# Optimization experiments

Hardware: AMD Instinct MI355X
Metric: run time of the kernel (lower is better)

Reference implementation:

```python
import jax, jax.numpy as jnp
import numpy as np

V, D, NH, L, T, B = 32000, 1024, 16, 6, 1024, 2
HS = D // NH
EPS = 1e-5


def setup_inputs() -> dict:
    key = jax.random.key(0)
    ks = jax.random.split(key, 20)
    s = 0.02
    inp = {
        'tokens': jax.random.randint(ks[0], (B, T), 0, V),
        'tok_emb': jax.random.normal(ks[1], (V, D), jnp.float32) * s,
        'pos_emb': jax.random.normal(ks[2], (T, D), jnp.float32) * s,
        'Wq': jax.random.normal(ks[3], (L, D, NH, HS), jnp.float32) * s,
        'Wk': jax.random.normal(ks[4], (L, D, NH, HS), jnp.float32) * s,
        'Wv': jax.random.normal(ks[5], (L, D, NH, HS), jnp.float32) * s,
        'Wo': jax.random.normal(ks[6], (L, D, D), jnp.float32) * s,
        'bo': jnp.zeros((L, D), jnp.float32),
        'ln1_s': jnp.ones((L, D), jnp.float32),
        'ln1_b': jnp.zeros((L, D), jnp.float32),
        'ln2_s': jnp.ones((L, D), jnp.float32),
        'ln2_b': jnp.zeros((L, D), jnp.float32),
        'W1': jax.random.normal(ks[7], (L, D, 4 * D), jnp.float32) * s,
        'b1': jnp.zeros((L, 4 * D), jnp.float32),
        'W2': jax.random.normal(ks[8], (L, 4 * D, D), jnp.float32) * s,
        'b2': jnp.zeros((L, D), jnp.float32),
        'lnf_s': jnp.ones((D,), jnp.float32),
        'lnf_b': jnp.zeros((D,), jnp.float32),
        'Wlm': jax.random.normal(ks[9], (D, V), jnp.float32) * s,
        'blm': jnp.zeros((V,), jnp.float32),
    }
    return inp


def _layernorm(x, scale, bias):
    m = jnp.mean(x, axis=-1, keepdims=True)
    v = jnp.mean(jnp.square(x - m), axis=-1, keepdims=True)
    return (x - m) * jax.lax.rsqrt(v + EPS) * scale + bias


def reference(tokens, tok_emb, pos_emb, Wq, Wk, Wv, Wo, bo,
              ln1_s, ln1_b, ln2_s, ln2_b, W1, b1, W2, b2,
              lnf_s, lnf_b, Wlm, blm):
    x = tok_emb[tokens] + pos_emb[None, :, :]  # [B,T,D]
    causal = jnp.tril(jnp.ones((T, T), bool))
    scale = HS ** -0.5
    for l in range(L):
        h = _layernorm(x, ln1_s[l], ln1_b[l])
        q = jnp.einsum('btd,dhe->bhte', h, Wq[l])
        k = jnp.einsum('btd,dhe->bhte', h, Wk[l])
        v = jnp.einsum('btd,dhe->bhte', h, Wv[l])
        wei = jnp.einsum('bhqe,bhke->bhqk', q, k) * scale
        wei = jnp.where(causal, wei, -jnp.inf)
        wei = jax.nn.softmax(wei, axis=-1)
        attn = jnp.einsum('bhqk,bhke->bhqe', wei, v)  # [B,NH,T,HS]
        attn = attn.transpose(0, 2, 1, 3).reshape(B, T, D)
        x = x + attn @ Wo[l] + bo[l]
        h = _layernorm(x, ln2_s[l], ln2_b[l])
        x = x + jax.nn.relu(h @ W1[l] + b1[l]) @ W2[l] + b2[l]
    x = _layernorm(x, lnf_s, lnf_b)
    logits = x @ Wlm + blm  # [B,T,V]
    return logits
```

## Files before the change

### kernel.cpp

```cpp
#include <hip/hip_runtime.h>
#include <hip/hip_bf16.h>
#include <stdint.h>

#define L_LAYERS 6
#define D_MODEL  1024
#define N_HEAD   16
#define H_SZ     64
#define T_SEQ    1024
#define B_BATCH  2
#define M_ROWS   2048
#define V_VOCAB  32000

typedef __attribute__((ext_vector_type(8))) short bf16x8;
typedef __attribute__((ext_vector_type(4))) short bf16x4;
typedef __attribute__((ext_vector_type(4))) float floatx4;

static __device__ __forceinline__ short f2bf(float f) {
  __hip_bfloat16 h = __float2bfloat16(f);
  return *reinterpret_cast<short*>(&h);
}

static __device__ __forceinline__ void lds_cp16(const void* g, void* l) {
  __builtin_amdgcn_global_load_lds(
      (const __attribute__((address_space(1))) uint32_t*)g,
      (__attribute__((address_space(3))) uint32_t*)l, 16, 0, 0);
}

#define WVM(n) asm volatile("s_waitcnt vmcnt(" #n ")" ::: "memory")
#define BARR __builtin_amdgcn_s_barrier()

__global__ __launch_bounds__(256) void transpose_cvt(const float* __restrict__ in,
                                                     short* __restrict__ out,
                                                     int R, int C,
                                                     long in_stride, long out_stride) {
  in  += (size_t)blockIdx.z * in_stride;
  out += (size_t)blockIdx.z * out_stride;
  __shared__ float tile[64][65];
  int rt = blockIdx.x, ct = blockIdx.y;
  int tid = threadIdx.x;
  int r0 = tid >> 4;
  int c0 = (tid & 15) << 2;
  const float* ip = in + (size_t)(rt * 64) * C + ct * 64;
#pragma unroll
  for (int p = 0; p < 4; ++p) {
    int r = r0 + (p << 4);
    float4 v = *(const float4*)(ip + (size_t)r * C + c0);
    tile[r][c0] = v.x; tile[r][c0 + 1] = v.y; tile[r][c0 + 2] = v.z; tile[r][c0 + 3] = v.w;
  }
  __syncthreads();
  short* op = out + (size_t)(ct * 64) * R + rt * 64;
#pragma unroll
  for (int p = 0; p < 4; ++p) {
    int c = r0 + (p << 4);
    bf16x4 s;
    s.x = f2bf(tile[c0 + 0][c]);
    s.y = f2bf(tile[c0 + 1][c]);
    s.z = f2bf(tile[c0 + 2][c]);
    s.w = f2bf(tile[c0 + 3][c]);
    *(bf16x4*)(op + (size_t)c * R + c0) = s;
  }
}

__global__ __launch_bounds__(256) void embed_kernel(const int* __restrict__ tokens,
                                                    const float* __restrict__ tok_emb,
                                                    const float* __restrict__ pos_emb,
                                                    float* __restrict__ x) {
  int row = blockIdx.x;
  int t = row & 1023;
  int tok = tokens[row];
  int c = threadIdx.x << 2;
  float4 e = *(const float4*)(tok_emb + (size_t)tok * 1024 + c);
  float4 p = *(const float4*)(pos_emb + (size_t)t * 1024 + c);
  float4 rr; rr.x = e.x + p.x; rr.y = e.y + p.y; rr.z = e.z + p.z; rr.w = e.w + p.w;
  *(float4*)(x + (size_t)row * 1024 + c) = rr;
}

__global__ __launch_bounds__(256) void ln_kernel(const float* __restrict__ xin,
                                                 const float* __restrict__ sc,
                                                 const float* __restrict__ bi,
                                                 short* __restrict__ out) {
  int row = blockIdx.x, tid = threadIdx.x;
  int c = tid << 2;
  float4 v = *(const float4*)(xin + (size_t)row * 1024 + c);
  float s = v.x + v.y + v.z + v.w;
  float q = v.x * v.x + v.y * v.y + v.z * v.z + v.w * v.w;
#pragma unroll
  for (int off = 32; off > 0; off >>= 1) {
    s += __shfl_xor(s, off);
    q += __shfl_xor(q, off);
  }
  __shared__ float rs[4], rq[4];
  if ((tid & 63) == 0) { rs[tid >> 6] = s; rq[tid >> 6] = q; }
  __syncthreads();
  s = rs[0] + rs[1] + rs[2] + rs[3];
  q = rq[0] + rq[1] + rq[2] + rq[3];
  float mean = s * (1.f / 1024.f);
  float var = q * (1.f / 1024.f) - mean * mean;
  float rstd = rsqrtf(var + 1e-5f);
  float4 g = *(const float4*)(sc + c);
  float4 bb = *(const float4*)(bi + c);
  bf16x4 o4;
  o4.x = f2bf((v.x - mean) * rstd * g.x + bb.x);
  o4.y = f2bf((v.y - mean) * rstd * g.y + bb.y);
  o4.z = f2bf((v.z - mean) * rstd * g.z + bb.z);
  o4.w = f2bf((v.w - mean) * rstd * g.w + bb.w);
  *(bf16x4*)(out + (size_t)row * 1024 + c) = o4;
}

__global__ __launch_bounds__(256) void lnred_kernel(float* __restrict__ xio,
                                                    const float* __restrict__ P0,
                                                    const float* __restrict__ P1,
                                                    const float* __restrict__ gb,
                                                    const float* __restrict__ sc,
                                                    const float* __restrict__ bi,
                                                    short* __restrict__ out) {
  int row = blockIdx.x, tid = threadIdx.x;
  int c = tid << 2;
  size_t base = (size_t)row * 1024 + c;
  float4 v = *(const float4*)(xio + base);
  float4 p0 = *(const float4*)(P0 + base);
  float4 p1 = *(const float4*)(P1 + base);
  float4 gv = *(const float4*)(gb + c);
  v.x += p0.x + p1.x + gv.x;
  v.y += p0.y + p1.y + gv.y;
  v.z += p0.z + p1.z + gv.z;
  v.w += p0.w + p1.w + gv.w;
  *(float4*)(xio + base) = v;
  float s = v.x + v.y + v.z + v.w;
  float q = v.x * v.x + v.y * v.y + v.z * v.z + v.w * v.w;
#pragma unroll
  for (int off = 32; off > 0; off >>= 1) {
    s += __shfl_xor(s, off);
    q += __shfl_xor(q, off);
  }
  __shared__ float rs[4], rq[4];
  if ((tid & 63) == 0) { rs[tid >> 6] = s; rq[tid >> 6] = q; }
  __syncthreads();
  s = rs[0] + rs[1] + rs[2] + rs[3];
  q = rq[0] + rq[1] + rq[2] + rq[3];
  float mean = s * (1.f / 1024.f);
  float var = q * (1.f / 1024.f) - mean * mean;
  float rstd = rsqrtf(var + 1e-5f);
  float4 g = *(const float4*)(sc + c);
  float4 bb = *(const float4*)(bi + c);
  bf16x4 o4;
  o4.x = f2bf((v.x - mean) * rstd * g.x + bb.x);
  o4.y = f2bf((v.y - mean) * rstd * g.y + bb.y);
  o4.z = f2bf((v.z - mean) * rstd * g.z + bb.z);
  o4.w = f2bf((v.w - mean) * rstd * g.w + bb.w);
  *(bf16x4*)(out + (size_t)row * 1024 + c) = o4;
}

template <bool BIAS, bool RELU, bool RESID, bool OUTBF16>
__global__ __launch_bounds__(256) void gemm3_kernel(const short* __restrict__ A,
                                                    const short* __restrict__ Bt,
                                                    const float* __restrict__ bias,
                                                    const float* __restrict__ resid,
                                                    void* __restrict__ Cout,
                                                    int K, int N) {
  constexpr int ABY = 64 * 128;
  constexpr int BBY = 128 * 128;
  extern __shared__ char smem[];
  char* Asm = smem;
  char* Bsm = smem + 3 * ABY;
  const int NB = N >> 7;
  int nwg = 32 * NB;
  int bid = blockIdx.x;
  int wgid = (bid & 7) * (nwg >> 3) + (bid >> 3);
  int bn = wgid >> 5, bm = wgid & 31;
  int tid = threadIdx.x;
  int lane = tid & 63, w = tid >> 6;
  int lr = lane & 15, lg = lane >> 4;
  int wn = w & 1, wm = w >> 1;

  const floatx4 FZ = {0.f, 0.f, 0.f, 0.f};
  floatx4 acc[2][4];
#pragma unroll
  for (int m = 0; m < 2; ++m)
#pragma unroll
    for (int n = 0; n < 4; ++n) acc[m][n] = FZ;

  size_t aoff[2], boff[4];
  {
    int rr = tid >> 3;
    int g = (tid & 7) ^ (rr & 7);
#pragma unroll
    for (int i = 0; i < 2; ++i)
      aoff[i] = (size_t)(bm * 64 + i * 32 + rr) * K + g * 8;
#pragma unroll
    for (int i = 0; i < 4; ++i)
      boff[i] = (size_t)(bn * 128 + i * 32 + rr) * K + g * 8;
  }

#define STA3(b, k0)                                                        \
  _Pragma("unroll") for (int i = 0; i < 2; ++i)                            \
    lds_cp16(A + aoff[i] + (k0), Asm + (b) * ABY + i * 4096 + tid * 16);
#define STB3(b, k0)                                                        \
  _Pragma("unroll") for (int i = 0; i < 4; ++i)                            \
    lds_cp16(Bt + boff[i] + (k0), Bsm + (b) * BBY + i * 4096 + tid * 16);
#define LDA3(b, kh)                                                        \
  _Pragma("unroll") for (int f = 0; f < 2; ++f) {                          \
    int lrow = wm * 32 + f * 16 + lr;                                      \
    af[f] = *(const bf16x8*)(Asm + (b) * ABY + lrow * 128 +                \
                             (((((kh) << 2) + lg) ^ (lrow & 7)) << 4));    \
  }
#define LDB3(b, kh)                                                        \
  _Pragma("unroll") for (int n = 0; n < 4; ++n) {                          \
    int lcol = wn * 64 + n * 16 + lr;                                      \
    bfr[n] = *(const bf16x8*)(Bsm + (b) * BBY + lcol * 128 +               \
                              (((((kh) << 2) + lg) ^ (lcol & 7)) << 4));   \
  }
#define MFMA3                                                              \
  __builtin_amdgcn_s_setprio(1);                                           \
  _Pragma("unroll") for (int f = 0; f < 2; ++f)                            \
  _Pragma("unroll") for (int n = 0; n < 4; ++n)                            \
    acc[f][n] = __builtin_amdgcn_mfma_f32_16x16x32_bf16(af[f], bfr[n],     \
                                                        acc[f][n], 0, 0, 0);\
  __builtin_amdgcn_s_setprio(0);

  const int nt = K >> 6;
  STA3(0, 0); STB3(0, 0);
  STA3(1, 64); STB3(1, 64);
  WVM(6);
  BARR;

  int cbuf = 0, sbuf = 2;
  for (int t = 0; t < nt; ++t) {
    bf16x8 af[2], bfr[4];
    bool pre = (t + 2 < nt);
    int k2 = (t + 2) << 6;
    if (pre) { STA3(sbuf, k2); }
    LDA3(cbuf, 0); LDB3(cbuf, 0);
    MFMA3;
    if (pre) { STB3(sbuf, k2); }
    LDA3(cbuf, 1); LDB3(cbuf, 1);
    MFMA3;
    if (pre) { WVM(6); } else { WVM(0); }
    BARR;
    cbuf = (cbuf == 2) ? 0 : cbuf + 1;
    sbuf = (sbuf == 2) ? 0 : sbuf + 1;
  }

#pragma unroll
  for (int n = 0; n < 4; ++n) {
    int col = (bn << 7) + wn * 64 + (n << 4) + lr;
    float bv = 0.f;
    if (BIAS) bv = bias[col];
#pragma unroll
    for (int m = 0; m < 2; ++m) {
      int row0 = bm * 64 + wm * 32 + (m << 4) + (lg << 2);
#pragma unroll
      for (int r = 0; r < 4; ++r) {
        size_t idx = (size_t)(row0 + r) * N + col;
        float val = acc[m][n][r] + bv;
        if (RESID) val += resid[idx];
        if (RELU) val = fmaxf(val, 0.f);
        if (OUTBF16) ((short*)Cout)[idx] = f2bf(val);
        else ((float*)Cout)[idx] = val;
      }
    }
  }
#undef STA3
#undef STB3
#undef LDA3
#undef LDB3
#undef MFMA3
}

__global__ __launch_bounds__(256) void gemm3sk_kernel(const short* __restrict__ A,
                                                      const short* __restrict__ Bt,
                                                      float* __restrict__ Pout,
                                                      int K, int N) {
  constexpr int ABY = 64 * 128;
  constexpr int BBY = 128 * 128;
  extern __shared__ char smem[];
  char* Asm = smem;
  char* Bsm = smem + 3 * ABY;
  const int NB = N >> 7;
  int nwg = 64 * NB;
  int bid = blockIdx.x;
  int wgid = (bid & 7) * (nwg >> 3) + (bid >> 3);
  int half = wgid >= (nwg >> 1);
  int w2 = wgid - half * (nwg >> 1);
  int bn = w2 >> 5, bm = w2 & 31;
  int kbase = half * (K >> 1);
  Pout += (size_t)half * M_ROWS * N;
  int tid = threadIdx.x;
  int lane = tid & 63, w = tid >> 6;
  int lr = lane & 15, lg = lane >> 4;
  int wn = w & 1, wm = w >> 1;

  const floatx4 FZ = {0.f, 0.f, 0.f, 0.f};
  floatx4 acc[2][4];
#pragma unroll
  for (int m = 0; m < 2; ++m)
#pragma unroll
    for (int n = 0; n < 4; ++n) acc[m][n] = FZ;

  size_t aoff[2], boff[4];
  {
    int rr = tid >> 3;
    int g = (tid & 7) ^ (rr & 7);
#pragma unroll
    for (int i = 0; i < 2; ++i)
      aoff[i] = (size_t)(bm * 64 + i * 32 + rr) * K + kbase + g * 8;
#pragma unroll
    for (int i = 0; i < 4; ++i)
      boff[i] = (size_t)(bn * 128 + i * 32 + rr) * K + kbase + g * 8;
  }

#define STA3(b, k0)                                                        \
  _Pragma("unroll") for (int i = 0; i < 2; ++i)                            \
    lds_cp16(A + aoff[i] + (k0), Asm + (b) * ABY + i * 4096 + tid * 16);
#define STB3(b, k0)                                                        \
  _Pragma("unroll") for (int i = 0; i < 4; ++i)                            \
    lds_cp16(Bt + boff[i] + (k0), Bsm + (b) * BBY + i * 4096 + tid * 16);
#define LDA3(b, kh)                                                        \
  _Pragma("unroll") for (int f = 0; f < 2; ++f) {                          \
    int lrow = wm * 32 + f * 16 + lr;                                      \
    af[f] = *(const bf16x8*)(Asm + (b) * ABY + lrow * 128 +                \
                             (((((kh) << 2) + lg) ^ (lrow & 7)) << 4));    \
  }
#define LDB3(b, kh)                                                        \
  _Pragma("unroll") for (int n = 0; n < 4; ++n) {                          \
    int lcol = wn * 64 + n * 16 + lr;                                      \
    bfr[n] = *(const bf16x8*)(Bsm + (b) * BBY + lcol * 128 +               \
                              (((((kh) << 2) + lg) ^ (lcol & 7)) << 4));   \
  }
#define MFMA3                                                              \
  __builtin_amdgcn_s_setprio(1);                                           \
  _Pragma("unroll") for (int f = 0; f < 2; ++f)                            \
  _Pragma("unroll") for (int n = 0; n < 4; ++n)                            \
    acc[f][n] = __builtin_amdgcn_mfma_f32_16x16x32_bf16(af[f], bfr[n],     \
                                                        acc[f][n], 0, 0, 0);\
  __builtin_amdgcn_s_setprio(0);

  const int nt = (K >> 1) >> 6;
  STA3(0, 0); STB3(0, 0);
  STA3(1, 64); STB3(1, 64);
  WVM(6);
  BARR;

  int cbuf = 0, sbuf = 2;
  for (int t = 0; t < nt; ++t) {
    bf16x8 af[2], bfr[4];
    bool pre = (t + 2 < nt);
    int k2 = (t + 2) << 6;
    if (pre) { STA3(sbuf, k2); }
    LDA3(cbuf, 0); LDB3(cbuf, 0);
    MFMA3;
    if (pre) { STB3(sbuf, k2); }
    LDA3(cbuf, 1); LDB3(cbuf, 1);
    MFMA3;
    if (pre) { WVM(6); } else { WVM(0); }
    BARR;
    cbuf = (cbuf == 2) ? 0 : cbuf + 1;
    sbuf = (sbuf == 2) ? 0 : sbuf + 1;
  }

#pragma unroll
  for (int n = 0; n < 4; ++n) {
    int col = (bn << 7) + wn * 64 + (n << 4) + lr;
#pragma unroll
    for (int m = 0; m < 2; ++m) {
      int row0 = bm * 64 + wm * 32 + (m << 4) + (lg << 2);
#pragma unroll
      for (int r = 0; r < 4; ++r)
        Pout[(size_t)(row0 + r) * N + col] = acc[m][n][r];
    }
  }
#undef STA3
#undef STB3
#undef LDA3
#undef LDB3
#undef MFMA3
}

template <bool BIAS, bool RELU, bool OUTBF16>
__global__ __launch_bounds__(512) void gemmw_kernel(const short* __restrict__ A,
                                                    const short* __restrict__ Bt,
                                                    const float* __restrict__ bias,
                                                    void* __restrict__ Cout,
                                                    int K, int N) {
  constexpr int ABY = 128 * 128;
  constexpr int BBY = 256 * 128;
  extern __shared__ char smem[];
  char* Asm = smem;
  char* Bsm = smem + 3 * ABY;
  const int NB = N >> 8;
  int nwg = 16 * NB;
  int bid = blockIdx.x;
  int wgid = (bid & 7) * (nwg >> 3) + (bid >> 3);
  int bn = wgid >> 4, bm = wgid & 15;
  int tid = threadIdx.x;
  int lane = tid & 63, w = tid >> 6;
  int lr = lane & 15, lg = lane >> 4;
  int wm = w >> 2, wn = w & 3;

  const floatx4 FZ = {0.f, 0.f, 0.f, 0.f};
  floatx4 acc[4][4];
#pragma unroll
  for (int m = 0; m < 4; ++m)
#pragma unroll
    for (int n = 0; n < 4; ++n) acc[m][n] = FZ;

  size_t aoff[2], boff[4];
  {
    int rr = tid >> 3;
    int g = (tid & 7) ^ (rr & 7);
#pragma unroll
    for (int i = 0; i < 2; ++i)
      aoff[i] = (size_t)(bm * 128 + i * 64 + rr) * K + g * 8;
#pragma unroll
    for (int i = 0; i < 4; ++i)
      boff[i] = (size_t)(bn * 256 + i * 64 + rr) * K + g * 8;
  }

#define STAW(b, k0)                                                        \
  _Pragma("unroll") for (int i = 0; i < 2; ++i)                            \
    lds_cp16(A + aoff[i] + (k0), Asm + (b) * ABY + i * 8192 + tid * 16);
#define STBW(b, k0)                                                        \
  _Pragma("unroll") for (int i = 0; i < 4; ++i)                            \
    lds_cp16(Bt + boff[i] + (k0), Bsm + (b) * BBY + i * 8192 + tid * 16);
#define LDAW(b, kh)                                                        \
  _Pragma("unroll") for (int f = 0; f < 4; ++f) {                          \
    int lrow = wm * 64 + f * 16 + lr;                                      \
    af[f] = *(const bf16x8*)(Asm + (b) * ABY + lrow * 128 +                \
                             (((((kh) << 2) + lg) ^ (lrow & 7)) << 4));    \
  }
#define LDBW(b, kh)                                                        \
  _Pragma("unroll") for (int n = 0; n < 4; ++n) {                          \
    int lcol = wn * 64 + n * 16 + lr;                                      \
    bfr[n] = *(const bf16x8*)(Bsm + (b) * BBY + lcol * 128 +               \
                              (((((kh) << 2) + lg) ^ (lcol & 7)) << 4));   \
  }
#define MFMAW                                                              \
  __builtin_amdgcn_s_setprio(1);                                           \
  _Pragma("unroll") for (int f = 0; f < 4; ++f)                            \
  _Pragma("unroll") for (int n = 0; n < 4; ++n)                            \
    acc[f][n] = __builtin_amdgcn_mfma_f32_16x16x32_bf16(af[f], bfr[n],     \
                                                        acc[f][n], 0, 0, 0);\
  __builtin_amdgcn_s_setprio(0);

  const int nt = K >> 6;
  STAW(0, 0); STBW(0, 0);
  STAW(1, 64); STBW(1, 64);
  WVM(6);
  BARR;

  int cbuf = 0, sbuf = 2;
  for (int t = 0; t < nt; ++t) {
    bf16x8 af[4], bfr[4];
    bool pre = (t + 2 < nt);
    int k2 = (t + 2) << 6;
    if (pre) { STAW(sbuf, k2); }
    LDAW(cbuf, 0); LDBW(cbuf, 0);
    MFMAW;
    if (pre) { STBW(sbuf, k2); }
    LDAW(cbuf, 1); LDBW(cbuf, 1);
    MFMAW;
    if (pre) { WVM(6); } else { WVM(0); }
    BARR;
    cbuf = (cbuf == 2) ? 0 : cbuf + 1;
    sbuf = (sbuf == 2) ? 0 : sbuf + 1;
  }

#pragma unroll
  for (int n = 0; n < 4; ++n) {
    int col = (bn << 8) + wn * 64 + (n << 4) + lr;
    float bv = 0.f;
    if (BIAS) bv = bias[col];
#pragma unroll
    for (int m = 0; m < 4; ++m) {
      int row0 = bm * 128 + wm * 64 + (m << 4) + (lg << 2);
#pragma unroll
      for (int r = 0; r < 4; ++r) {
        size_t idx = (size_t)(row0 + r) * N + col;
        float val = acc[m][n][r] + bv;
        if (RELU) val = fmaxf(val, 0.f);
        if (OUTBF16) ((short*)Cout)[idx] = f2bf(val);
        else ((float*)Cout)[idx] = val;
      }
    }
  }
#undef STAW
#undef STBW
#undef LDAW
#undef LDBW
#undef MFMAW
}

template <bool BIAS, bool OUTBF16>
__global__ __launch_bounds__(512) void gemm8_kernel(const short* __restrict__ A,
                                                    const short* __restrict__ Bt,
                                                    const float* __restrict__ bias,
                                                    void* __restrict__ Cout,
                                                    int K, int N) {
  extern __shared__ char smem[];
  char* Asm = smem;
  char* Bsm = smem + 65536;
  const int NB = N >> 8;
  int nwg = 8 * NB;
  int bid = blockIdx.x;
  int wgid = (bid & 7) * (nwg >> 3) + (bid >> 3);
  int bm = wgid & 7, bn = wgid >> 3;
  int tid = threadIdx.x;
  int lane = tid & 63, w = tid >> 6;
  int lr = lane & 15, lg = lane >> 4;
  int wm = w >> 2, wn = w & 3;

  const floatx4 FZ = {0.f, 0.f, 0.f, 0.f};
  floatx4 acc[8][4];
#pragma unroll
  for (int m = 0; m < 8; ++m)
#pragma unroll
    for (int n = 0; n < 4; ++n) acc[m][n] = FZ;

  size_t aoff[2][2], boff[4];
  {
    int rr = tid >> 3;
    int g = (tid & 7) ^ (rr & 7);
#pragma unroll
    for (int c = 0; c < 2; ++c)
#pragma unroll
      for (int i = 0; i < 2; ++i) {
        int lrow = i * 64 + rr;
        int grow = (lrow & 63) + ((lrow >> 6) << 7) + (c << 6);
        aoff[c][i] = (size_t)(bm * 256 + grow) * K + g * 8;
      }
#pragma unroll
    for (int i = 0; i < 4; ++i)
      boff[i] = (size_t)(bn * 256 + i * 64 + rr) * K + g * 8;
  }

  bf16x8 areg[4], breg[2][4];

#define LDA8(chunk, kh)                                                          \
  _Pragma("unroll") for (int f = 0; f < 4; ++f) {                                \
    int lrow = wm * 64 + f * 16 + lr;                                            \
    areg[f] = *(const bf16x8*)(Asm + buf * 32768 + (chunk) * 16384 + lrow * 128  \
                               + (((((kh) << 2) + lg) ^ (lrow & 7)) << 4));      \
  }
#define LDB8(kh)                                                                 \
  _Pragma("unroll") for (int n = 0; n < 4; ++n) {                                \
    int lcol = wn * 64 + n * 16 + lr;                                            \
    breg[kh][n] = *(const bf16x8*)(Bsm + buf * 32768 + lcol * 128                \
                                   + (((((kh) << 2) + lg) ^ (lcol & 7)) << 4));  \
  }
#define MFMA16(mh, kh)                                                           \
  __builtin_amdgcn_s_setprio(1);                                                 \
  _Pragma("unroll") for (int f = 0; f < 4; ++f)                                  \
  _Pragma("unroll") for (int n = 0; n < 4; ++n)                                  \
    acc[(mh) * 4 + f][n] = __builtin_amdgcn_mfma_f32_16x16x32_bf16(              \
        areg[f], breg[kh][n], acc[(mh) * 4 + f][n], 0, 0, 0);                    \
  __builtin_amdgcn_s_setprio(0);
#define STA8(chunk, dstbuf, k0)                                                  \
  _Pragma("unroll") for (int i = 0; i < 2; ++i)                                  \
    lds_cp16(A + aoff[chunk][i] + (k0),                                          \
             Asm + (dstbuf) * 32768 + (chunk) * 16384 + i * 8192 + tid * 16);
#define STB8(dstbuf, k0)                                                         \
  _Pragma("unroll") for (int i = 0; i < 4; ++i)                                  \
    lds_cp16(Bt + boff[i] + (k0),                                                \
             Bsm + (dstbuf) * 32768 + i * 8192 + tid * 16);

  const int nt = K >> 6;
  STA8(0, 0, 0); STB8(0, 0); STA8(1, 0, 0);
  WVM(2);
  BARR;

  int buf = 0;
  for (int t = 0; t < nt - 1; ++t) {
    int k1 = (t + 1) << 6;
    int ob = buf ^ 1;
    LDA8(0, 0); LDB8(0);
    STA8(0, ob, k1);
    BARR;
    MFMA16(0, 0);
    BARR;
    LDA8(0, 1); LDB8(1);
    STB8(ob, k1);
    WVM(6);
    BARR;
    MFMA16(0, 1);
    BARR;
    LDA8(1, 0);
    STA8(1, ob, k1);
    BARR;
    MFMA16(1, 0);
    BARR;
    LDA8(1, 1);
    WVM(2);
    BARR;
    MFMA16(1, 1);
    BARR;
    buf ^= 1;
  }
  LDA8(0, 0); LDB8(0);
  MFMA16(0, 0);
  LDA8(0, 1); LDB8(1);
  MFMA16(0, 1);
  WVM(0);
  BARR;
  LDA8(1, 0);
  MFMA16(1, 0);
  LDA8(1, 1);
  MFMA16(1, 1);

#pragma unroll
  for (int n = 0; n < 4; ++n) {
    int col = (bn << 8) + (wn << 6) + (n << 4) + lr;
    float bv = 0.f;
    if (BIAS) bv = bias[col];
#pragma unroll
    for (int m = 0; m < 8; ++m) {
      int row0 = (bm << 8) + (wm << 7) + (m << 4) + (lg << 2);
#pragma unroll
      for (int r = 0; r < 4; ++r) {
        size_t idx = (size_t)(row0 + r) * N + col;
        float val = acc[m][n][r] + bv;
        if (OUTBF16) ((short*)Cout)[idx] = f2bf(val);
        else ((float*)Cout)[idx] = val;
      }
    }
  }
#undef LDA8
#undef LDB8
#undef MFMA16
#undef STA8
#undef STB8
}

__global__ __launch_bounds__(256) void vt_kernel(const short* __restrict__ qkv,
                                                 short* __restrict__ vt) {
  int bh = blockIdx.x, tt = blockIdx.y;
  int b = bh >> 4, hh = bh & 15;
  __shared__ short tile[64][68];
  int tid = threadIdx.x;
  int r0 = tid >> 4;
  int c4 = (tid & 15) << 2;
  const short* ip = qkv + (size_t)((b << 10) + (tt << 6)) * 3072 + 2048 + (hh << 6);
#pragma unroll
  for (int p = 0; p < 4; ++p) {
    int t = r0 + (p << 4);
    bf16x4 v = *(const bf16x4*)(ip + (size_t)t * 3072 + c4);
    tile[t][c4] = v.x; tile[t][c4 + 1] = v.y; tile[t][c4 + 2] = v.z; tile[t][c4 + 3] = v.w;
  }
  __syncthreads();
  short* op = vt + (size_t)(bh << 6) * 1024 + (tt << 6);
#pragma unroll
  for (int p = 0; p < 4; ++p) {
    int e = r0 + (p << 4);
    bf16x4 sv;
    sv.x = tile[c4 + 0][e];
    sv.y = tile[c4 + 1][e];
    sv.z = tile[c4 + 2][e];
    sv.w = tile[c4 + 3][e];
    *(bf16x4*)(op + (size_t)e * 1024 + c4) = sv;
  }
}

__global__ __launch_bounds__(256) void attn_kernel(const short* __restrict__ qkv,
                                                   const short* __restrict__ vt,
                                                   short* __restrict__ out) {
  int bh = blockIdx.x;
  int qt = blockIdx.y;
  int b = bh >> 4, hh = bh & 15;
  int tid = threadIdx.x;
  int lane = tid & 63, w = tid >> 6;
  int lr = lane & 15, lg = lane >> 4;

  __shared__ short Ks[64 * 64];
  __shared__ short Vs[64 * 64];
  __shared__ short Ps[4][16 * 68];

  const floatx4 FZ = {0.f, 0.f, 0.f, 0.f};
  const short* qb = qkv + (size_t)((b << 10) + (qt << 6) + (w << 4) + lr) * 3072 + (hh << 6);
  bf16x8 qf0 = *(const bf16x8*)(qb + (lg << 3));
  bf16x8 qf1 = *(const bf16x8*)(qb + 32 + (lg << 3));

  floatx4 o[4];
  float mrun[4], lrun[4];
#pragma unroll
  for (int r = 0; r < 4; ++r) { o[r] = FZ; mrun[r] = -3e38f; lrun[r] = 0.f; }

  int sr = lane >> 3;
  int cb = (lane & 7) << 4;
  int csw = cb ^ (sr << 4);
  const short* kB = qkv + (size_t)(b << 10) * 3072 + 1024 + (hh << 6);
  const short* vB = vt + (size_t)(bh << 6) * 1024;

  for (int jt = 0; jt <= qt; ++jt) {
    __syncthreads();
#pragma unroll
    for (int j = 0; j < 2; ++j) {
      int ch = w * 2 + j;
      int row = (ch << 3) + sr;
      lds_cp16(kB + (size_t)((jt << 6) + row) * 3072 + (csw >> 1), (short*)Ks + (ch << 9));
      lds_cp16(vB + (size_t)row * 1024 + (jt << 6) + (csw >> 1), (short*)Vs + (ch << 9));
    }
    __syncthreads();

    const char* KsB = (const char*)Ks;
    const char* VsB = (const char*)Vs;
    floatx4 s[4];
#pragma unroll
    for (int f = 0; f < 4; ++f) {
      int rk = (f << 4) + lr;
      int sw = (rk & 7) << 4;
      bf16x8 kf0 = *(const bf16x8*)(KsB + rk * 128 + ((lg << 4) ^ sw));
      bf16x8 kf1 = *(const bf16x8*)(KsB + rk * 128 + ((64 + (lg << 4)) ^ sw));
      floatx4 t = __builtin_amdgcn_mfma_f32_16x16x32_bf16(qf0, kf0, FZ, 0, 0, 0);
      s[f] = __builtin_amdgcn_mfma_f32_16x16x32_bf16(qf1, kf1, t, 0, 0, 0);
    }

    float p[4][4], mt[4];
    bool diag = (jt == qt);
    int rowloc = (w << 4) + (lg << 2);
#pragma unroll
    for (int r = 0; r < 4; ++r) {
      float m = -3e38f;
#pragma unroll
      for (int f = 0; f < 4; ++f) {
        float sv = s[f][r] * 0.125f;
        if (diag && ((f << 4) + lr > rowloc + r)) sv = -3e38f;
        p[f][r] = sv;
        m = fmaxf(m, sv);
      }
      mt[r] = m;
    }
#pragma unroll
    for (int off = 1; off < 16; off <<= 1) {
#pragma unroll
      for (int r = 0; r < 4; ++r) mt[r] = fmaxf(mt[r], __shfl_xor(mt[r], off));
    }
    float corr[4], psum[4];
#pragma unroll
    for (int r = 0; r < 4; ++r) {
      float mnew = fmaxf(mrun[r], mt[r]);
      corr[r] = __expf(mrun[r] - mnew);
      mrun[r] = mnew;
      float ps = 0.f;
#pragma unroll
      for (int f = 0; f < 4; ++f) {
        float e = __expf(p[f][r] - mnew);
        p[f][r] = e;
        ps += e;
      }
      psum[r] = ps;
    }
#pragma unroll
    for (int off = 1; off < 16; off <<= 1) {
#pragma unroll
      for (int r = 0; r < 4; ++r) psum[r] += __shfl_xor(psum[r], off);
    }
    floatx4 cv;
#pragma unroll
    for (int r = 0; r < 4; ++r) { lrun[r] = lrun[r] * corr[r] + psum[r]; cv[r] = corr[r]; }
#pragma unroll
    for (int f = 0; f < 4; ++f) o[f] *= cv;

    char* PsB = (char*)&Ps[w][0];
#pragma unroll
    for (int f = 0; f < 4; ++f)
#pragma unroll
      for (int r = 0; r < 4; ++r)
        *(short*)(PsB + ((lg << 2) + r) * 136 + (((f << 4) + lr) << 1)) = f2bf(p[f][r]);

#pragma unroll
    for (int kk = 0; kk < 2; ++kk) {
      const char* pb = PsB + lr * 136 + (kk << 6) + (lg << 4);
      union { struct { bf16x4 lo, hi; } h2; bf16x8 v; } pu;
      pu.h2.lo = *(const bf16x4*)pb;
      pu.h2.hi = *(const bf16x4*)(pb + 8);
      bf16x8 pa = pu.v;
#pragma unroll
      for (int f = 0; f < 4; ++f) {
        int rv = (f << 4) + lr;
        int sw = (rv & 7) << 4;
        bf16x8 vf = *(const bf16x8*)(VsB + rv * 128 + ((((kk << 6)) + (lg << 4)) ^ sw));
        o[f] = __builtin_amdgcn_mfma_f32_16x16x32_bf16(pa, vf, o[f], 0, 0, 0);
      }
    }
  }

#pragma unroll
  for (int f = 0; f < 4; ++f) {
#pragma unroll
    for (int r = 0; r < 4; ++r) {
      int row = (qt << 6) + (w << 4) + (lg << 2) + r;
      int col = (hh << 6) + (f << 4) + lr;
      out[(size_t)((b << 10) + row) * 1024 + col] = f2bf(o[f][r] / lrun[r]);
    }
  }
}

extern "C" void kernel_launch(void* const* d_in, const int* in_sizes, int n_in,
                              void* d_out, int out_size, void* d_ws, size_t ws_size,
                              hipStream_t stream) {
  const int*   tokens  = (const int*)d_in[0];
  const float* tok_emb = (const float*)d_in[1];
  const float* pos_emb = (const float*)d_in[2];
  const float* Wq  = (const float*)d_in[3];
  const float* Wk  = (const float*)d_in[4];
  const float* Wv  = (const float*)d_in[5];
  const float* Wo  = (const float*)d_in[6];
  const float* bo  = (const float*)d_in[7];
  const float* ln1s = (const float*)d_in[8];
  const float* ln1b = (const float*)d_in[9];
  const float* ln2s = (const float*)d_in[10];
  const float* ln2b = (const float*)d_in[11];
  const float* W1  = (const float*)d_in[12];
  const float* b1  = (const float*)d_in[13];
  const float* W2  = (const float*)d_in[14];
  const float* b2  = (const float*)d_in[15];
  const float* lnfs = (const float*)d_in[16];
  const float* lnfb = (const float*)d_in[17];
  const float* Wlm = (const float*)d_in[18];
  const float* blm = (const float*)d_in[19];

  short* wqkvT = (short*)d_ws;
  short* woT   = wqkvT + (size_t)L_LAYERS * 3072 * 1024;
  short* w1T   = woT   + (size_t)L_LAYERS * 1024 * 1024;
  short* w2T   = w1T   + (size_t)L_LAYERS * 4096 * 1024;
  short* wlmT  = w2T   + (size_t)L_LAYERS * 1024 * 4096;
  float* x     = (float*)(wlmT + (size_t)V_VOCAB * 1024);
  short* h     = (short*)(x + (size_t)M_ROWS * 1024);
  short* qkv   = h + (size_t)M_ROWS * 1024;
  short* vtb   = qkv + (size_t)M_ROWS * 3072;
  short* attnb = vtb + (size_t)B_BATCH * N_HEAD * H_SZ * T_SEQ;
  short* mid   = attnb + (size_t)M_ROWS * 1024;
  float* psum  = (float*)(mid + (size_t)M_ROWS * 4096);
  float* psum1 = psum + (size_t)M_ROWS * 1024;

  dim3 blk(256, 1, 1);

  (void)hipFuncSetAttribute(reinterpret_cast<const void*>(&gemm8_kernel<true, false>),
                            hipFuncAttributeMaxDynamicSharedMemorySize, 131072);
  (void)hipFuncSetAttribute(reinterpret_cast<const void*>(&gemm3_kernel<false, false, false, true>),
                            hipFuncAttributeMaxDynamicSharedMemorySize, 73728);
  (void)hipFuncSetAttribute(reinterpret_cast<const void*>(&gemm3sk_kernel),
                            hipFuncAttributeMaxDynamicSharedMemorySize, 73728);
  (void)hipFuncSetAttribute(reinterpret_cast<const void*>(&gemmw_kernel<true, true, true>),
                            hipFuncAttributeMaxDynamicSharedMemorySize, 147456);

  transpose_cvt<<<dim3(16, 16, 6), blk, 0, stream>>>(Wq, wqkvT,             1024, 1024, 1048576, 3072 * 1024);
  transpose_cvt<<<dim3(16, 16, 6), blk, 0, stream>>>(Wk, wqkvT + 1048576,   1024, 1024, 1048576, 3072 * 1024);
  transpose_cvt<<<dim3(16, 16, 6), blk, 0, stream>>>(Wv, wqkvT + 2097152,   1024, 1024, 1048576, 3072 * 1024);
  transpose_cvt<<<dim3(16, 16, 6), blk, 0, stream>>>(Wo, woT,               1024, 1024, 1048576, 1048576);
  transpose_cvt<<<dim3(16, 64, 6), blk, 0, stream>>>(W1, w1T,               1024, 4096, 4194304, 4194304);
  transpose_cvt<<<dim3(64, 16, 6), blk, 0, stream>>>(W2, w2T,               4096, 1024, 4194304, 4194304);
  transpose_cvt<<<dim3(16, 500, 1), blk, 0, stream>>>(Wlm, wlmT,            1024, V_VOCAB, 0, 0);

  embed_kernel<<<M_ROWS, blk, 0, stream>>>(tokens, tok_emb, pos_emb, x);

  for (int l = 0; l < L_LAYERS; ++l) {
    if (l == 0) {
      ln_kernel<<<M_ROWS, blk, 0, stream>>>(x, ln1s, ln1b, h);
    } else {
      lnred_kernel<<<M_ROWS, blk, 0, stream>>>(x, psum, psum1, b2 + (l - 1) * 1024,
                                               ln1s + l * 1024, ln1b + l * 1024, h);
    }
    gemm3_kernel<false, false, false, true><<<32 * 24, blk, 73728, stream>>>(
        h, wqkvT + (size_t)l * 3072 * 1024, nullptr, nullptr, qkv, 1024, 3072);
    vt_kernel<<<dim3(32, 16), blk, 0, stream>>>(qkv, vtb);
    attn_kernel<<<dim3(32, 16), blk, 0, stream>>>(qkv, vtb, attnb);
    gemm3sk_kernel<<<64 * 8, blk, 73728, stream>>>(
        attnb, woT + (size_t)l * 1048576, psum, 1024, 1024);
    lnred_kernel<<<M_ROWS, blk, 0, stream>>>(x, psum, psum1, bo + l * 1024,
                                             ln2s + l * 1024, ln2b + l * 1024, h);
    gemmw_kernel<true, true, true><<<16 * 16, dim3(512, 1, 1), 147456, stream>>>(
        h, w1T + (size_t)l * 4194304, b1 + l * 4096, mid, 1024, 4096);
    gemm3sk_kernel<<<64 * 8, blk, 73728, stream>>>(
        mid, w2T + (size_t)l * 4194304, psum, 4096, 1024);
  }

  lnred_kernel<<<M_ROWS, blk, 0, stream>>>(x, psum, psum1, b2 + 5 * 1024,
                                           lnfs, lnfb, h);
  gemm8_kernel<true, false><<<dim3(8 * 125), dim3(512, 1, 1), 131072, stream>>>(
      h, wlmT, blm, (float*)d_out, 1024, V_VOCAB);
}
```

Measured before the change: 1.141 ms.

## Use wide-tile GEMMs for QKV and 4-way split-K FC2, fuse embed with LN

The QKV projection moves from the 64x128-tile gemm3 kernel to the 128x256-tile, 512-thread gemmw kernel. FC2 moves to a new 4-way split-K wide-tile kernel whose partials land in psum and in the qkv buffer, which is reused as scratch. A new lnred4 kernel sums the four partials plus bias into the residual and applies layernorm. The embedding is also fused with the first layernorm, saving a launch and a reread of x. The aim is better data reuse and fewer launches, at the cost of extra partial-sum traffic and fewer workgroups for the QKV GEMM.

```diff
diff --git a/kernel.cpp b/kernel.cpp
--- a/kernel.cpp
+++ b/kernel.cpp
@@ -61,27 +61,21 @@
   }
 }
 
-__global__ __launch_bounds__(256) void embed_kernel(const int* __restrict__ tokens,
-                                                    const float* __restrict__ tok_emb,
-                                                    const float* __restrict__ pos_emb,
-                                                    float* __restrict__ x) {
-  int row = blockIdx.x;
+__global__ __launch_bounds__(256) void embedln_kernel(const int* __restrict__ tokens,
+                                                      const float* __restrict__ tok_emb,
+                                                      const float* __restrict__ pos_emb,
+                                                      float* __restrict__ x,
+                                                      const float* __restrict__ sc,
+                                                      const float* __restrict__ bi,
+                                                      short* __restrict__ out) {
+  int row = blockIdx.x, tid = threadIdx.x;
   int t = row & 1023;
   int tok = tokens[row];
-  int c = threadIdx.x << 2;
+  int c = tid << 2;
   float4 e = *(const float4*)(tok_emb + (size_t)tok * 1024 + c);
   float4 p = *(const float4*)(pos_emb + (size_t)t * 1024 + c);
-  float4 rr; rr.x = e.x + p.x; rr.y = e.y + p.y; rr.z = e.z + p.z; rr.w = e.w + p.w;
-  *(float4*)(x + (size_t)row * 1024 + c) = rr;
-}
-
-__global__ __launch_bounds__(256) void ln_kernel(const float* __restrict__ xin,
-                                                 const float* __restrict__ sc,
-                                                 const float* __restrict__ bi,
-                                                 short* __restrict__ out) {
-  int row = blockIdx.x, tid = threadIdx.x;
-  int c = tid << 2;
-  float4 v = *(const float4*)(xin + (size_t)row * 1024 + c);
+  float4 v; v.x = e.x + p.x; v.y = e.y + p.y; v.z = e.z + p.z; v.w = e.w + p.w;
+  *(float4*)(x + (size_t)row * 1024 + c) = v;
   float s = v.x + v.y + v.z + v.w;
   float q = v.x * v.x + v.y * v.y + v.z * v.z + v.w * v.w;
 #pragma unroll
@@ -151,120 +145,51 @@
   *(bf16x4*)(out + (size_t)row * 1024 + c) = o4;
 }
 
-template <bool BIAS, bool RELU, bool RESID, bool OUTBF16>
-__global__ __launch_bounds__(256) void gemm3_kernel(const short* __restrict__ A,
-                                                    const short* __restrict__ Bt,
-                                                    const float* __restrict__ bias,
-                                                    const float* __restrict__ resid,
-                                                    void* __restrict__ Cout,
-                                                    int K, int N) {
-  constexpr int ABY = 64 * 128;
-  constexpr int BBY = 128 * 128;
-  extern __shared__ char smem[];
-  char* Asm = smem;
-  char* Bsm = smem + 3 * ABY;
-  const int NB = N >> 7;
-  int nwg = 32 * NB;
-  int bid = blockIdx.x;
-  int wgid = (bid & 7) * (nwg >> 3) + (bid >> 3);
-  int bn = wgid >> 5, bm = wgid & 31;
-  int tid = threadIdx.x;
-  int lane = tid & 63, w = tid >> 6;
-  int lr = lane & 15, lg = lane >> 4;
-  int wn = w & 1, wm = w >> 1;
-
-  const floatx4 FZ = {0.f, 0.f, 0.f, 0.f};
-  floatx4 acc[2][4];
-#pragma unroll
-  for (int m = 0; m < 2; ++m)
-#pragma unroll
-    for (int n = 0; n < 4; ++n) acc[m][n] = FZ;
-
-  size_t aoff[2], boff[4];
-  {
-    int rr = tid >> 3;
-    int g = (tid & 7) ^ (rr & 7);
-#pragma unroll
-    for (int i = 0; i < 2; ++i)
-      aoff[i] = (size_t)(bm * 64 + i * 32 + rr) * K + g * 8;
-#pragma unroll
-    for (int i = 0; i < 4; ++i)
-      boff[i] = (size_t)(bn * 128 + i * 32 + rr) * K + g * 8;
-  }
-
-#define STA3(b, k0)                                                        \
-  _Pragma("unroll") for (int i = 0; i < 2; ++i)                            \
-    lds_cp16(A + aoff[i] + (k0), Asm + (b) * ABY + i * 4096 + tid * 16);
-#define STB3(b, k0)                                                        \
-  _Pragma("unroll") for (int i = 0; i < 4; ++i)                            \
-    lds_cp16(Bt + boff[i] + (k0), Bsm + (b) * BBY + i * 4096 + tid * 16);
-#define LDA3(b, kh)                                                        \
-  _Pragma("unroll") for (int f = 0; f < 2; ++f) {                          \
-    int lrow = wm * 32 + f * 16 + lr;                                      \
-    af[f] = *(const bf16x8*)(Asm + (b) * ABY + lrow * 128 +                \
-                             (((((kh) << 2) + lg) ^ (lrow & 7)) << 4));    \
-  }
-#define LDB3(b, kh)                                                        \
-  _Pragma("unroll") for (int n = 0; n < 4; ++n) {                          \
-    int lcol = wn * 64 + n * 16 + lr;                                      \
-    bfr[n] = *(const bf16x8*)(Bsm + (b) * BBY + lcol * 128 +               \
-                              (((((kh) << 2) + lg) ^ (lcol & 7)) << 4));   \
-  }
-#define MFMA3                                                              \
-  __builtin_amdgcn_s_setprio(1);                                           \
-  _Pragma("unroll") for (int f = 0; f < 2; ++f)                            \
-  _Pragma("unroll") for (int n = 0; n < 4; ++n)                            \
-    acc[f][n] = __builtin_amdgcn_mfma_f32_16x16x32_bf16(af[f], bfr[n],     \
-                                                        acc[f][n], 0, 0, 0);\
-  __builtin_amdgcn_s_setprio(0);
-
-  const int nt = K >> 6;
-  STA3(0, 0); STB3(0, 0);
-  STA3(1, 64); STB3(1, 64);
-  WVM(6);
-  BARR;
-
-  int cbuf = 0, sbuf = 2;
-  for (int t = 0; t < nt; ++t) {
-    bf16x8 af[2], bfr[4];
-    bool pre = (t + 2 < nt);
-    int k2 = (t + 2) << 6;
-    if (pre) { STA3(sbuf, k2); }
-    LDA3(cbuf, 0); LDB3(cbuf, 0);
-    MFMA3;
-    if (pre) { STB3(sbuf, k2); }
-    LDA3(cbuf, 1); LDB3(cbuf, 1);
-    MFMA3;
-    if (pre) { WVM(6); } else { WVM(0); }
-    BARR;
-    cbuf = (cbuf == 2) ? 0 : cbuf + 1;
-    sbuf = (sbuf == 2) ? 0 : sbuf + 1;
-  }
-
-#pragma unroll
-  for (int n = 0; n < 4; ++n) {
-    int col = (bn << 7) + wn * 64 + (n << 4) + lr;
-    float bv = 0.f;
-    if (BIAS) bv = bias[col];
-#pragma unroll
-    for (int m = 0; m < 2; ++m) {
-      int row0 = bm * 64 + wm * 32 + (m << 4) + (lg << 2);
-#pragma unroll
-      for (int r = 0; r < 4; ++r) {
-        size_t idx = (size_t)(row0 + r) * N + col;
-        float val = acc[m][n][r] + bv;
-        if (RESID) val += resid[idx];
-        if (RELU) val = fmaxf(val, 0.f);
-        if (OUTBF16) ((short*)Cout)[idx] = f2bf(val);
-        else ((float*)Cout)[idx] = val;
-      }
-    }
-  }
-#undef STA3
-#undef STB3
-#undef LDA3
-#undef LDB3
-#undef MFMA3
+__global__ __launch_bounds__(256) void lnred4_kernel(float* __restrict__ xio,
+                                                     const float* __restrict__ P01,
+                                                     const float* __restrict__ P23,
+                                                     const float* __restrict__ gb,
+                                                     const float* __restrict__ sc,
+                                                     const float* __restrict__ bi,
+                                                     short* __restrict__ out) {
+  const size_t MN = (size_t)M_ROWS * 1024;
+  int row = blockIdx.x, tid = threadIdx.x;
+  int c = tid << 2;
+  size_t base = (size_t)row * 1024 + c;
+  float4 v = *(const float4*)(xio + base);
+  float4 p0 = *(const float4*)(P01 + base);
+  float4 p1 = *(const float4*)(P01 + MN + base);
+  float4 p2 = *(const float4*)(P23 + base);
+  float4 p3 = *(const float4*)(P23 + MN + base);
+  float4 gv = *(const float4*)(gb + c);
+  v.x += p0.x + p1.x + p2.x + p3.x + gv.x;
+  v.y += p0.y + p1.y + p2.y + p3.y + gv.y;
+  v.z += p0.z + p1.z + p2.z + p3.z + gv.z;
+  v.w += p0.w + p1.w + p2.w + p3.w + gv.w;
+  *(float4*)(xio + base) = v;
+  float s = v.x + v.y + v.z + v.w;
+  float q = v.x * v.x + v.y * v.y + v.z * v.z + v.w * v.w;
+#pragma unroll
+  for (int off = 32; off > 0; off >>= 1) {
+    s += __shfl_xor(s, off);
+    q += __shfl_xor(q, off);
+  }
+  __shared__ float rs[4], rq[4];
+  if ((tid & 63) == 0) { rs[tid >> 6] = s; rq[tid >> 6] = q; }
+  __syncthreads();
+  s = rs[0] + rs[1] + rs[2] + rs[3];
+  q = rq[0] + rq[1] + rq[2] + rq[3];
+  float mean = s * (1.f / 1024.f);
+  float var = q * (1.f / 1024.f) - mean * mean;
+  float rstd = rsqrtf(var + 1e-5f);
+  float4 g = *(const float4*)(sc + c);
+  float4 bb = *(const float4*)(bi + c);
+  bf16x4 o4;
+  o4.x = f2bf((v.x - mean) * rstd * g.x + bb.x);
+  o4.y = f2bf((v.y - mean) * rstd * g.y + bb.y);
+  o4.z = f2bf((v.z - mean) * rstd * g.z + bb.z);
+  o4.w = f2bf((v.w - mean) * rstd * g.w + bb.w);
+  *(bf16x4*)(out + (size_t)row * 1024 + c) = o4;
 }
 
 __global__ __launch_bounds__(256) void gemm3sk_kernel(const short* __restrict__ A,
@@ -481,6 +406,118 @@
         if (OUTBF16) ((short*)Cout)[idx] = f2bf(val);
         else ((float*)Cout)[idx] = val;
       }
+    }
+  }
+#undef STAW
+#undef STBW
+#undef LDAW
+#undef LDBW
+#undef MFMAW
+}
+
+__global__ __launch_bounds__(512) void gemmwsk_kernel(const short* __restrict__ A,
+                                                      const short* __restrict__ Bt,
+                                                      float* __restrict__ P01,
+                                                      float* __restrict__ P23,
+                                                      int K, int N) {
+  constexpr int ABY = 128 * 128;
+  constexpr int BBY = 256 * 128;
+  extern __shared__ char smem[];
+  char* Asm = smem;
+  char* Bsm = smem + 3 * ABY;
+  const int NB = N >> 8;
+  int nwg = 16 * NB * 4;
+  int bid = blockIdx.x;
+  int wgid = (bid & 7) * (nwg >> 3) + (bid >> 3);
+  int per = nwg >> 2;
+  int part = wgid / per;
+  int w2 = wgid - part * per;
+  int bn = w2 >> 4, bm = w2 & 15;
+  int kbase = part * (K >> 2);
+  float* Pout = (part < 2 ? P01 + (size_t)part * M_ROWS * N
+                          : P23 + (size_t)(part - 2) * M_ROWS * N);
+  int tid = threadIdx.x;
+  int lane = tid & 63, w = tid >> 6;
+  int lr = lane & 15, lg = lane >> 4;
+  int wm = w >> 2, wn = w & 3;
+
+  const floatx4 FZ = {0.f, 0.f, 0.f, 0.f};
+  floatx4 acc[4][4];
+#pragma unroll
+  for (int m = 0; m < 4; ++m)
+#pragma unroll
+    for (int n = 0; n < 4; ++n) acc[m][n] = FZ;
+
+  size_t aoff[2], boff[4];
+  {
+    int rr = tid >> 3;
+    int g = (tid & 7) ^ (rr & 7);
+#pragma unroll
+    for (int i = 0; i < 2; ++i)
+      aoff[i] = (size_t)(bm * 128 + i * 64 + rr) * K + kbase + g * 8;
+#pragma unroll
+    for (int i = 0; i < 4; ++i)
+      boff[i] = (size_t)(bn * 256 + i * 64 + rr) * K + kbase + g * 8;
+  }
+
+#define STAW(b, k0)                                                        \
+  _Pragma("unroll") for (int i = 0; i < 2; ++i)                            \
+    lds_cp16(A + aoff[i] + (k0), Asm + (b) * ABY + i * 8192 + tid * 16);
+#define STBW(b, k0)                                                        \
+  _Pragma("unroll") for (int i = 0; i < 4; ++i)                            \
+    lds_cp16(Bt + boff[i] + (k0), Bsm + (b) * BBY + i * 8192 + tid * 16);
+#define LDAW(b, kh)                                                        \
+  _Pragma("unroll") for (int f = 0; f < 4; ++f) {                          \
+    int lrow = wm * 64 + f * 16 + lr;                                      \
+    af[f] = *(const bf16x8*)(Asm + (b) * ABY + lrow * 128 +                \
+                             (((((kh) << 2) + lg) ^ (lrow & 7)) << 4));    \
+  }
+#define LDBW(b, kh)                                                        \
+  _Pragma("unroll") for (int n = 0; n < 4; ++n) {                          \
+    int lcol = wn * 64 + n * 16 + lr;                                      \
+    bfr[n] = *(const bf16x8*)(Bsm + (b) * BBY + lcol * 128 +               \
+                              (((((kh) << 2) + lg) ^ (lcol & 7)) << 4));   \
+  }
+#define MFMAW                                                              \
+  __builtin_amdgcn_s_setprio(1);                                           \
+  _Pragma("unroll") for (int f = 0; f < 4; ++f)                            \
+  _Pragma("unroll") for (int n = 0; n < 4; ++n)                            \
+    acc[f][n] = __builtin_amdgcn_mfma_f32_16x16x32_bf16(af[f], bfr[n],     \
+                                                        acc[f][n], 0, 0, 0);\
+  __builtin_amdgcn_s_setprio(0);
+
+  const int nt = (K >> 2) >> 6;
+  STAW(0, 0); STBW(0, 0);
+  STAW(1, 64); STBW(1, 64);
+  WVM(6);
+  BARR;
+
+  int cbuf = 0, sbuf = 2;
+  for (int t = 0; t < nt; ++t) {
+    bf16x8 af[4], bfr[4];
+    bool pre = (t + 2 < nt);
+    int k2 = (t + 2) << 6;
+    if (pre) { STAW(sbuf, k2); }
+    LDAW(cbuf, 0); LDBW(cbuf, 0);
+    MFMAW;
+    if (pre) { STBW(sbuf, k2); }
+    LDAW(cbuf, 1); LDBW(cbuf, 1);
+    MFMAW;
+    if (pre) { WVM(6); } else { WVM(0); }
+    BARR;
+    cbuf = (cbuf == 2) ? 0 : cbuf + 1;
+    sbuf = (sbuf == 2) ? 0 : sbuf + 1;
+  }
+
+#pragma unroll
+  for (int n = 0; n < 4; ++n) {
+    int col = (bn << 8) + wn * 64 + (n << 4) + lr;
+#pragma unroll
+    for (int m = 0; m < 4; ++m) {
+      int row0 = bm * 128 + wm * 64 + (m << 4) + (lg << 2);
+#pragma unroll
+      for (int r = 0; r < 4; ++r)
+        Pout[(size_t)(row0 + r) * N + col] = acc[m][n][r];
     }
   }
 #undef STAW
@@ -831,16 +868,19 @@
   short* mid   = attnb + (size_t)M_ROWS * 1024;
   float* psum  = (float*)(mid + (size_t)M_ROWS * 4096);
   float* psum1 = psum + (size_t)M_ROWS * 1024;
+  float* psum23 = (float*)qkv;
 
   dim3 blk(256, 1, 1);
 
   (void)hipFuncSetAttribute(reinterpret_cast<const void*>(&gemm8_kernel<true, false>),
                             hipFuncAttributeMaxDynamicSharedMemorySize, 131072);
-  (void)hipFuncSetAttribute(reinterpret_cast<const void*>(&gemm3_kernel<false, false, false, true>),
-                            hipFuncAttributeMaxDynamicSharedMemorySize, 73728);
   (void)hipFuncSetAttribute(reinterpret_cast<const void*>(&gemm3sk_kernel),
                             hipFuncAttributeMaxDynamicSharedMemorySize, 73728);
+  (void)hipFuncSetAttribute(reinterpret_cast<const void*>(&gemmw_kernel<false, false, true>),
+                            hipFuncAttributeMaxDynamicSharedMemorySize, 147456);
   (void)hipFuncSetAttribute(reinterpret_cast<const void*>(&gemmw_kernel<true, true, true>),
+                            hipFuncAttributeMaxDynamicSharedMemorySize, 147456);
+  (void)hipFuncSetAttribute(reinterpret_cast<const void*>(&gemmwsk_kernel),
                             hipFuncAttributeMaxDynamicSharedMemorySize, 147456);
 
   transpose_cvt<<<dim3(16, 16, 6), blk, 0, stream>>>(Wq, wqkvT,             1024, 1024, 1048576, 3072 * 1024);
@@ -851,17 +891,15 @@
   transpose_cvt<<<dim3(64, 16, 6), blk, 0, stream>>>(W2, w2T,               4096, 1024, 4194304, 4194304);
   transpose_cvt<<<dim3(16, 500, 1), blk, 0, stream>>>(Wlm, wlmT,            1024, V_VOCAB, 0, 0);
 
-  embed_kernel<<<M_ROWS, blk, 0, stream>>>(tokens, tok_emb, pos_emb, x);
+  embedln_kernel<<<M_ROWS, blk, 0, stream>>>(tokens, tok_emb, pos_emb, x, ln1s, ln1b, h);
 
   for (int l = 0; l < L_LAYERS; ++l) {
-    if (l == 0) {
-      ln_kernel<<<M_ROWS, blk, 0, stream>>>(x, ln1s, ln1b, h);
-    } else {
-      lnred_kernel<<<M_ROWS, blk, 0, stream>>>(x, psum, psum1, b2 + (l - 1) * 1024,
-                                               ln1s + l * 1024, ln1b + l * 1024, h);
-    }
-    gemm3_kernel<false, false, false, true><<<32 * 24, blk, 73728, stream>>>(
-        h, wqkvT + (size_t)l * 3072 * 1024, nullptr, nullptr, qkv, 1024, 3072);
+    if (l > 0) {
+      lnred4_kernel<<<M_ROWS, blk, 0, stream>>>(x, psum, psum23, b2 + (l - 1) * 1024,
+                                                ln1s + l * 1024, ln1b + l * 1024, h);
+    }
+    gemmw_kernel<false, false, true><<<16 * 12, dim3(512, 1, 1), 147456, stream>>>(
+        h, wqkvT + (size_t)l * 3072 * 1024, nullptr, qkv, 1024, 3072);
     vt_kernel<<<dim3(32, 16), blk, 0, stream>>>(qkv, vtb);
     attn_kernel<<<dim3(32, 16), blk, 0, stream>>>(qkv, vtb, attnb);
     gemm3sk_kernel<<<64 * 8, blk, 73728, stream>>>(
@@ -870,12 +908,12 @@
                                              ln2s + l * 1024, ln2b + l * 1024, h);
     gemmw_kernel<true, true, true><<<16 * 16, dim3(512, 1, 1), 147456, stream>>>(
         h, w1T + (size_t)l * 4194304, b1 + l * 4096, mid, 1024, 4096);
-    gemm3sk_kernel<<<64 * 8, blk, 73728, stream>>>(
-        mid, w2T + (size_t)l * 4194304, psum, 4096, 1024);
-  }
-
-  lnred_kernel<<<M_ROWS, blk, 0, stream>>>(x, psum, psum1, b2 + 5 * 1024,
-                                           lnfs, lnfb, h);
+    gemmwsk_kernel<<<16 * 16, dim3(512, 1, 1), 147456, stream>>>(
+        mid, w2T + (size_t)l * 4194304, psum, psum23, 4096, 1024);
+  }
+
+  lnred4_kernel<<<M_ROWS, blk, 0, stream>>>(x, psum, psum23, b2 + 5 * 1024,
+                                            lnfs, lnfb, h);
   gemm8_kernel<true, false><<<dim3(8 * 125), dim3(512, 1, 1), 131072, stream>>>(
       h, wlmT, blm, (float*)d_out, 1024, V_VOCAB);
 }
```

After: 1.075 ms. 5.8% less time.
